# Optimization experiments

Measured on AMD Instinct MI355X. Metric: run time of the kernel, lower is better.

## Reference

```python
import jax, jax.numpy as jnp
import numpy as np

EMBED, ACT, DETER, STOCH, HID = 1536, 10, 2048, 64, 1024
T, B = 64, 256
LN_EPS = 1e-3


def _ln(x, s, b):
    mu = jnp.mean(x, axis=-1, keepdims=True)
    var = jnp.mean(jnp.square(x - mu), axis=-1, keepdims=True)
    return (x - mu) * jax.lax.rsqrt(var + LN_EPS) * s + b


def setup_inputs() -> dict:
    key = jax.random.key(0)
    ks = jax.random.split(key, 20)
    g = lambda k, shp, fan: jax.random.normal(k, shp, jnp.float32) * (1.0 / np.sqrt(fan))
    inp = {
        "embeds": jax.random.normal(ks[0], (T, B, EMBED), jnp.float32),
        "actions": jax.random.normal(ks[1], (T, B, ACT), jnp.float32),
        "h_t": jnp.zeros((B, DETER), jnp.float32),
        "z_t": jnp.zeros((B, STOCH), jnp.float32),
        "noise": jax.random.normal(ks[2], (T, B, STOCH), jnp.float32),
        # DeterNext
        "z_mlp_w": g(ks[3], (HID // 2, STOCH), STOCH),
        "z_mlp_b": jnp.zeros((HID // 2,), jnp.float32),
        "a_mlp_w": g(ks[4], (HID // 2, ACT), ACT),  # bias=False
        "ln_za_s": jnp.ones((HID,), jnp.float32),
        "ln_za_b": jnp.zeros((HID,), jnp.float32),
        # GRUCell (torch layout: [3*deter, in])
        "gru_wih": g(ks[5], (3 * DETER, HID), HID),
        "gru_whh": g(ks[6], (3 * DETER, DETER), DETER),
        "gru_bih": jnp.zeros((3 * DETER,), jnp.float32),
        "gru_bhh": jnp.zeros((3 * DETER,), jnp.float32),
        # PosteriorNext
        "post_h_w": g(ks[7], (HID, DETER), DETER),
        "post_h_b": jnp.zeros((HID,), jnp.float32),
        "post_e_w": g(ks[8], (HID, EMBED), EMBED),
        "post_e_b": jnp.zeros((HID,), jnp.float32),
        "ln_post_s": jnp.ones((HID,), jnp.float32),
        "ln_post_b": jnp.zeros((HID,), jnp.float32),
        "post_w": g(ks[9], (2 * STOCH, HID), HID),
        "post_b": jnp.zeros((2 * STOCH,), jnp.float32),
        # PriorNext
        "prior_h_w": g(ks[10], (HID, DETER), DETER),
        "prior_h_b": jnp.zeros((HID,), jnp.float32),
        "ln_prior_s": jnp.ones((HID,), jnp.float32),
        "ln_prior_b": jnp.zeros((HID,), jnp.float32),
        "prior_w": g(ks[11], (2 * STOCH, HID), HID),
        "prior_b": jnp.zeros((2 * STOCH,), jnp.float32),
    }
    return inp


def _rssm_forward(embeds, actions, h0, z0, noise,
                  z_mlp_w, z_mlp_b, a_mlp_w, ln_za_s, ln_za_b,
                  gru_wih, gru_whh, gru_bih, gru_bhh,
                  post_h_w, post_h_b, post_e_w, post_e_b, ln_post_s, ln_post_b,
                  post_w, post_b,
                  prior_h_w, prior_h_b, ln_prior_s, ln_prior_b, prior_w, prior_b):
    def step(carry, xs):
        h, z = carry
        e, a, n = xs
        # DeterNext: concat(z_mlp(z), a_mlp(a)) -> LN -> ELU
        x = jnp.concatenate([z @ z_mlp_w.T + z_mlp_b, a @ a_mlp_w.T], axis=-1)
        za = jax.nn.elu(_ln(x, ln_za_s, ln_za_b))
        # GRUCell
        gi = za @ gru_wih.T + gru_bih
        gh = h @ gru_whh.T + gru_bhh
        ir, iu, ic = jnp.split(gi, 3, axis=-1)
        hr, hu, hc = jnp.split(gh, 3, axis=-1)
        r = jax.nn.sigmoid(ir + hr)
        u = jax.nn.sigmoid(iu + hu)
        c = jnp.tanh(ic + r * hc)
        h1 = (1.0 - u) * c + u * h
        # PosteriorNext
        p = jax.nn.elu(_ln(h1 @ post_h_w.T + post_h_b + e @ post_e_w.T + post_e_b,
                           ln_post_s, ln_post_b))
        post = p @ post_w.T + post_b  # [B, 2*stoch]
        mean, sraw = jnp.split(post, 2, axis=-1)
        std = 2.0 * jax.nn.sigmoid(sraw) + 0.1
        z1 = mean + std * n  # rsample with externally-supplied noise
        return (h1, z1), (post, h1, z1)

    (_, _), (posts, states_h, post_z_samples) = jax.lax.scan(
        step, (h0, z0), (embeds, actions, noise))
    # batch prior over all timesteps
    pr = jax.nn.elu(_ln(states_h @ prior_h_w.T + prior_h_b, ln_prior_s, ln_prior_b))
    priors = pr @ prior_w.T + prior_b  # [T, B, 2*stoch]
    features = jnp.concatenate([states_h, post_z_samples], axis=-1)  # [T,B,deter+stoch]
    return priors, posts, post_z_samples, features


def reference(embeds, actions, h_t, z_t, noise,
              z_mlp_w, z_mlp_b, a_mlp_w, ln_za_s, ln_za_b,
              gru_wih, gru_whh, gru_bih, gru_bhh,
              post_h_w, post_h_b, post_e_w, post_e_b, ln_post_s, ln_post_b,
              post_w, post_b,
              prior_h_w, prior_h_b, ln_prior_s, ln_prior_b, prior_w, prior_b):
    return _rssm_forward(embeds, actions, h_t, z_t, noise,
                         z_mlp_w, z_mlp_b, a_mlp_w, ln_za_s, ln_za_b,
                         gru_wih, gru_whh, gru_bih, gru_bhh,
                         post_h_w, post_h_b, post_e_w, post_e_b, ln_post_s, ln_post_b,
                         post_w, post_b,
                         prior_h_w, prior_h_b, ln_prior_s, ln_prior_b, prior_w, prior_b)
```

## Files before the change

kernel.cpp:

```cpp
#include <hip/hip_runtime.h>

#define LN_EPS 1e-3f

typedef short s8v __attribute__((ext_vector_type(8)));
typedef float f4v __attribute__((ext_vector_type(4)));
typedef unsigned short u16;

__device__ __forceinline__ u16 f2bf(float f) {
  unsigned int x = __float_as_uint(f);
  x += 0x7fffu + ((x >> 16) & 1u);
  return (u16)(x >> 16);
}
__device__ __forceinline__ float bf2f(u16 u) {
  return __uint_as_float(((unsigned int)u) << 16);
}

__device__ __forceinline__ void glds16(const u16* g, void* l) {
  __builtin_amdgcn_global_load_lds(
      (const __attribute__((address_space(1))) void*)g,
      (__attribute__((address_space(3))) void*)l, 16, 0, 0);
}

__global__ void k_cvt(const float* __restrict__ src, u16* __restrict__ dst, int n) {
  int i = blockIdx.x * blockDim.x + threadIdx.x;
  int stride = gridDim.x * blockDim.x;
  for (; i < n; i += stride) dst[i] = f2bf(src[i]);
}

__global__ void k_packgru(const float* __restrict__ wih,
                          const float* __restrict__ whh, u16* __restrict__ wt) {
  int u = blockIdx.x * 256 + threadIdx.x;
  int nt = u / 73728;
  int r1 = u % 73728;
  int s = r1 / 1536;
  int r2 = r1 % 1536;
  int sub = r2 / 512;
  int r3 = r2 % 512;
  int ch = r3 / 64;
  int row = r3 % 64;
  int j = nt * 64 + row;
  int kbase = s * 64 + ch * 8;
  s8v v;
#pragma unroll
  for (int e = 0; e < 8; ++e) {
    int kk = kbase + e;
    float x;
    if (sub == 0) {
      x = kk < 1024 ? wih[(size_t)j * 1024 + kk] : whh[(size_t)j * 2048 + kk - 1024];
    } else if (sub == 1) {
      int jj = 2048 + j;
      x = kk < 1024 ? wih[(size_t)jj * 1024 + kk] : whh[(size_t)jj * 2048 + kk - 1024];
    } else {
      int jj = 4096 + j;
      x = (s < 16) ? wih[(size_t)jj * 1024 + kk] : whh[(size_t)jj * 2048 + kk - 1024];
    }
    v[e] = (short)f2bf(x);
  }
  *(s8v*)(wt + (size_t)u * 8) = v;
}

__global__ void k_packB(const float* __restrict__ src, u16* __restrict__ dst,
                        int K, int BN, int total) {
  int u = blockIdx.x * 256 + threadIdx.x;
  if (u >= total) return;
  int ns = K >> 6;
  int perNt = ns * 8 * BN;
  int nt = u / perNt;
  int r1 = u % perNt;
  int s = r1 / (8 * BN);
  int r2 = r1 % (8 * BN);
  int ch = r2 / BN;
  int row = r2 % BN;
  int j = nt * BN + row;
  int k = s * 64 + ch * 8;
  const float* sp = src + (size_t)j * K + k;
  s8v v;
#pragma unroll
  for (int e = 0; e < 8; ++e) v[e] = (short)f2bf(sp[e]);
  *(s8v*)(dst + (size_t)u * 8) = v;
}

__global__ void k_hinit(const float* __restrict__ h0, float* __restrict__ hf,
                        u16* __restrict__ acat) {
  int i = blockIdx.x * 256 + threadIdx.x;
  int b = i >> 11, j = i & 2047;
  float v = h0[i];
  hf[i] = v;
  acat[(size_t)b * 3072 + 1024 + j] = f2bf(v);
}

__global__ __launch_bounds__(256) void k_za(
    const float* __restrict__ zsrc, const float* __restrict__ act,
    const float* __restrict__ zw, const float* __restrict__ zb,
    const float* __restrict__ aw, const float* __restrict__ lns,
    const float* __restrict__ lnb, u16* __restrict__ acat) {
  const int b = blockIdx.x, tid = threadIdx.x;
  __shared__ float zsh[64];
  __shared__ float ash[12];
  __shared__ float wred[8];
  if (tid < 64) zsh[tid] = zsrc[b * 64 + tid];
  if (tid < 10) ash[tid] = act[b * 10 + tid];
  __syncthreads();
  float x[4];
#pragma unroll
  for (int i = 0; i < 2; ++i) {
    int c = tid + i * 256;
    const float4* wp = (const float4*)(zw + c * 64);
    float a = zb[c];
#pragma unroll
    for (int k = 0; k < 16; ++k) {
      float4 v = wp[k];
      a += zsh[k * 4] * v.x + zsh[k * 4 + 1] * v.y + zsh[k * 4 + 2] * v.z +
           zsh[k * 4 + 3] * v.w;
    }
    x[i] = a;
  }
#pragma unroll
  for (int i = 2; i < 4; ++i) {
    int c2 = tid + (i - 2) * 256;
    const float* wp = aw + c2 * 10;
    float a = 0.f;
#pragma unroll
    for (int k = 0; k < 10; ++k) a += ash[k] * wp[k];
    x[i] = a;
  }
  float s = x[0] + x[1] + x[2] + x[3];
#pragma unroll
  for (int o = 1; o < 64; o <<= 1) s += __shfl_xor(s, o);
  if ((tid & 63) == 0) wred[tid >> 6] = s;
  __syncthreads();
  float mu = (wred[0] + wred[1] + wred[2] + wred[3]) * (1.f / 1024.f);
  float q = 0.f;
#pragma unroll
  for (int i = 0; i < 4; ++i) {
    float d = x[i] - mu;
    q += d * d;
  }
#pragma unroll
  for (int o = 1; o < 64; o <<= 1) q += __shfl_xor(q, o);
  if ((tid & 63) == 0) wred[4 + (tid >> 6)] = q;
  __syncthreads();
  float rs = rsqrtf((wred[4] + wred[5] + wred[6] + wred[7]) * (1.f / 1024.f) + LN_EPS);
  int cols[4] = {tid, tid + 256, 512 + tid, 768 + tid};
#pragma unroll
  for (int i = 0; i < 4; ++i) {
    int c = cols[i];
    float y = (x[i] - mu) * rs * lns[c] + lnb[c];
    y = y > 0.f ? y : expm1f(y);
    acat[(size_t)b * 3072 + c] = f2bf(y);
  }
}

__global__ __launch_bounds__(256) void k_gru(
    const u16* __restrict__ acat_r, const u16* __restrict__ wt,
    const float* __restrict__ bih, const float* __restrict__ bhh,
    const float* __restrict__ hf_r, float* __restrict__ hf_w,
    u16* __restrict__ acat_w, float* __restrict__ feat, int t) {
  const int hw = blockIdx.x;
  const int logical = (hw & 7) * 32 + (hw >> 3);
  const int mg = logical & 7;
  const int nt = logical >> 3;
  const int m0 = mg * 32;
  const int tid = threadIdx.x;
  const int lane = tid & 63;
  const int w = tid >> 6;
  const int lr = lane & 15, lk = lane >> 4;

  __shared__ __align__(16) char smem[2][28672];

  const int arow = 8 * w + (lane >> 3);
  const int acol8 = ((lane & 7) ^ (arow & 7)) * 8;
  const u16* aSrc = acat_r + (size_t)(m0 + arow) * 3072 + acol8;
  const u16* wtNt = wt + (size_t)nt * 48 * 3 * 4096;

  f4v accr[2], accu[2], acci[2], acch[2];
  accr[0] = accr[1] = accu[0] = accu[1] = (f4v)(0.f);
  acci[0] = acci[1] = acch[0] = acch[1] = (f4v)(0.f);

#define K1_STAGE(BB, S) { \
    char* base = &smem[BB][0]; \
    glds16(aSrc + (S) * 64, base + w * 1024); \
    const u16* bsrc = wtNt + (size_t)(S) * 3 * 4096; \
    _Pragma("unroll") for (int i = 0; i < 6; ++i) { \
      int cf = w + i * 4; \
      glds16(bsrc + (cf * 64 + lane) * 8, base + 4096 + cf * 1024); \
    } }

#define K1_COMP(BB, ACCX) { \
    char* base = &smem[BB][0]; \
    _Pragma("unroll") for (int kk = 0; kk < 2; ++kk) { \
      int ch = kk * 4 + lk; \
      int r0 = lr, r1 = 16 + lr; \
      s8v a0 = *(const s8v*)(base + r0 * 128 + ((ch ^ (r0 & 7)) * 16)); \
      s8v a1 = *(const s8v*)(base + r1 * 128 + ((ch ^ (r1 & 7)) * 16)); \
      int rb = (w * 16 + lr) * 16; \
      s8v br = *(const s8v*)(base + 4096 + ch * 1024 + rb); \
      s8v bu = *(const s8v*)(base + 12288 + ch * 1024 + rb); \
      s8v bx = *(const s8v*)(base + 20480 + ch * 1024 + rb); \
      accr[0] = __builtin_amdgcn_mfma_f32_16x16x32_bf16(a0, br, accr[0], 0, 0, 0); \
      accr[1] = __builtin_amdgcn_mfma_f32_16x16x32_bf16(a1, br, accr[1], 0, 0, 0); \
      accu[0] = __builtin_amdgcn_mfma_f32_16x16x32_bf16(a0, bu, accu[0], 0, 0, 0); \
      accu[1] = __builtin_amdgcn_mfma_f32_16x16x32_bf16(a1, bu, accu[1], 0, 0, 0); \
      ACCX[0] = __builtin_amdgcn_mfma_f32_16x16x32_bf16(a0, bx, ACCX[0], 0, 0, 0); \
      ACCX[1] = __builtin_amdgcn_mfma_f32_16x16x32_bf16(a1, bx, ACCX[1], 0, 0, 0); \
    } }

  K1_STAGE(0, 0)
  int buf = 0;
  for (int s = 0; s < 16; ++s) {
    asm volatile("s_waitcnt vmcnt(0)" ::: "memory");
    __builtin_amdgcn_s_barrier();
    __builtin_amdgcn_sched_barrier(0);
    K1_STAGE(buf ^ 1, s + 1)
    K1_COMP(buf, acci)
    buf ^= 1;
  }
  for (int s = 16; s < 48; ++s) {
    asm volatile("s_waitcnt vmcnt(0)" ::: "memory");
    __builtin_amdgcn_s_barrier();
    __builtin_amdgcn_sched_barrier(0);
    if (s + 1 < 48) K1_STAGE(buf ^ 1, s + 1)
    K1_COMP(buf, acch)
    buf ^= 1;
  }

  const int j = nt * 64 + w * 16 + lr;
  const float b_ri = bih[j], b_rh = bhh[j];
  const float b_ui = bih[2048 + j], b_uh = bhh[2048 + j];
  const float b_ci = bih[4096 + j], b_ch = bhh[4096 + j];
#pragma unroll
  for (int m = 0; m < 2; ++m) {
#pragma unroll
    for (int r = 0; r < 4; ++r) {
      int grow = m0 + m * 16 + lk * 4 + r;
      float vr = accr[m][r] + b_ri + b_rh;
      float vu = accu[m][r] + b_ui + b_uh;
      float ic = acci[m][r] + b_ci;
      float hc = acch[m][r] + b_ch;
      float rg = 1.f / (1.f + expf(-vr));
      float ug = 1.f / (1.f + expf(-vu));
      float c = tanhf(ic + rg * hc);
      float hold = hf_r[(size_t)grow * 2048 + j];
      float h1 = (1.f - ug) * c + ug * hold;
      hf_w[(size_t)grow * 2048 + j] = h1;
      acat_w[(size_t)grow * 3072 + 1024 + j] = f2bf(h1);
      feat[(size_t)(t * 256 + grow) * 2112 + j] = h1;
    }
  }
#undef K1_STAGE
#undef K1_COMP
}

__global__ __launch_bounds__(256) void k_post(
    const u16* __restrict__ acat_h, const u16* __restrict__ wp,
    const float* __restrict__ bias, const u16* __restrict__ epart_t,
    float* __restrict__ xbuf) {
  const int bx = blockIdx.x;
  const int mg = bx & 7, nt = bx >> 3;
  const int m0 = mg * 32;
  const int tid = threadIdx.x;
  const int lane = tid & 63;
  const int w = tid >> 6;
  const int lr = lane & 15, lk = lane >> 4;

  __shared__ __align__(16) char smem[2][12288];

  const int arow = 8 * w + (lane >> 3);
  const int acol8 = ((lane & 7) ^ (arow & 7)) * 8;
  const u16* aSrc = acat_h + (size_t)(m0 + arow) * 3072 + 1024 + acol8;
  const u16* wpNt = wp + (size_t)nt * 32 * 4096;

  f4v acc[2];
  acc[0] = (f4v)(0.f);
  acc[1] = (f4v)(0.f);

#define K2_STAGE(BB, S) { \
    char* base = &smem[BB][0]; \
    glds16(aSrc + (S) * 64, base + w * 1024); \
    const u16* bsrc = wpNt + (size_t)(S) * 4096; \
    _Pragma("unroll") for (int i = 0; i < 2; ++i) { \
      int cf = w + i * 4; \
      glds16(bsrc + (cf * 64 + lane) * 8, base + 4096 + cf * 1024); \
    } }

  K2_STAGE(0, 0)
  int buf = 0;
  for (int s = 0; s < 32; ++s) {
    asm volatile("s_waitcnt vmcnt(0)" ::: "memory");
    __builtin_amdgcn_s_barrier();
    __builtin_amdgcn_sched_barrier(0);
    if (s + 1 < 32) K2_STAGE(buf ^ 1, s + 1)
    char* base = &smem[buf][0];
#pragma unroll
    for (int kk = 0; kk < 2; ++kk) {
      int ch = kk * 4 + lk;
      int r0 = lr, r1 = 16 + lr;
      s8v a0 = *(const s8v*)(base + r0 * 128 + ((ch ^ (r0 & 7)) * 16));
      s8v a1 = *(const s8v*)(base + r1 * 128 + ((ch ^ (r1 & 7)) * 16));
      s8v b = *(const s8v*)(base + 4096 + ch * 1024 + (w * 16 + lr) * 16);
      acc[0] = __builtin_amdgcn_mfma_f32_16x16x32_bf16(a0, b, acc[0], 0, 0, 0);
      acc[1] = __builtin_amdgcn_mfma_f32_16x16x32_bf16(a1, b, acc[1], 0, 0, 0);
    }
    buf ^= 1;
  }
  const int col = nt * 64 + w * 16 + lr;
#pragma unroll
  for (int m = 0; m < 2; ++m) {
#pragma unroll
    for (int r = 0; r < 4; ++r) {
      int grow = m0 + m * 16 + lk * 4 + r;
      float v = acc[m][r] + bias[col] + bf2f(epart_t[(size_t)grow * 1024 + col]);
      xbuf[(size_t)grow * 1024 + col] = v;
    }
  }
#undef K2_STAGE
}

__global__ __launch_bounds__(512) void k_postz(
    const float* __restrict__ xb, const u16* __restrict__ pw,
    const float* __restrict__ lns, const float* __restrict__ lnb,
    const float* __restrict__ pb, float* __restrict__ posts_t,
    const float* __restrict__ noise_t, float* __restrict__ zout,
    float* __restrict__ feat, int t) {
  const int m0 = blockIdx.x * 32;
  const int tid = threadIdx.x;
  const int lane = tid & 63;
  const int w = tid >> 6;
  const int lr = lane & 15, lk = lane >> 4;
  __shared__ __align__(16) u16 As[2][32][64];
  __shared__ __align__(16) u16 Bs[2][8][128][8];
  __shared__ float lmu[32], lrs[32];
  __shared__ float ps[32][132];
  {
    int row = tid >> 4, sg = tid & 15;
    const float4* xp = (const float4*)(xb + (size_t)(m0 + row) * 1024 + sg * 64);
    float s = 0.f, q = 0.f;
#pragma unroll
    for (int i = 0; i < 16; ++i) {
      float4 v = xp[i];
      s += v.x + v.y + v.z + v.w;
      q += v.x * v.x + v.y * v.y + v.z * v.z + v.w * v.w;
    }
#pragma unroll
    for (int o = 1; o < 16; o <<= 1) {
      s += __shfl_xor(s, o);
      q += __shfl_xor(q, o);
    }
    if (sg == 0) {
      float mu = s * (1.f / 1024.f);
      lmu[row] = mu;
      lrs[row] = rsqrtf(q * (1.f / 1024.f) - mu * mu + LN_EPS);
    }
  }
  __syncthreads();

#define K3_STAGEA(BB, S) if (tid < 256) { \
    int row = tid >> 3, k8 = tid & 7; \
    const float* xp = xb + (size_t)(m0 + row) * 1024 + (S) * 64 + k8 * 8; \
    float mu = lmu[row], rs = lrs[row]; \
    s8v v; \
    _Pragma("unroll") for (int e = 0; e < 8; ++e) { \
      int c = (S) * 64 + k8 * 8 + e; \
      float y = (xp[e] - mu) * rs * lns[c] + lnb[c]; \
      y = y > 0.f ? y : expm1f(y); \
      v[e] = (short)f2bf(y); \
    } \
    *(s8v*)((char*)&As[BB][0][0] + row * 128 + ((k8 ^ (row & 7)) * 16)) = v; }

#define K3_STAGEB(BB, S) { \
    const u16* bsrc = pw + (size_t)(S) * 8192; \
    glds16(bsrc + (((w >> 1) * 128 + (w & 1) * 64 + lane) * 8), \
           (char*)&Bs[BB][0][0][0] + w * 1024); \
    glds16(bsrc + ((((w >> 1) + 4) * 128 + (w & 1) * 64 + lane) * 8), \
           (char*)&Bs[BB][0][0][0] + w * 1024 + 8192); }

  f4v acc[2];
  acc[0] = (f4v)(0.f);
  acc[1] = (f4v)(0.f);
  K3_STAGEA(0, 0)
  K3_STAGEB(0, 0)
  __syncthreads();
  int buf = 0;
  for (int s = 0; s < 16; ++s) {
    if (s + 1 < 16) {
      K3_STAGEA(buf ^ 1, s + 1)
      K3_STAGEB(buf ^ 1, s + 1)
    }
#pragma unroll
    for (int kk = 0; kk < 2; ++kk) {
      int ch = kk * 4 + lk;
      int r0 = lr, r1 = 16 + lr;
      s8v a0 = *(const s8v*)((char*)&As[buf][0][0] + r0 * 128 + ((ch ^ (r0 & 7)) * 16));
      s8v a1 = *(const s8v*)((char*)&As[buf][0][0] + r1 * 128 + ((ch ^ (r1 & 7)) * 16));
      s8v b = *(const s8v*)((char*)&Bs[buf][0][0][0] + ch * 2048 + (w * 16 + lr) * 16);
      acc[0] = __builtin_amdgcn_mfma_f32_16x16x32_bf16(a0, b, acc[0], 0, 0, 0);
      acc[1] = __builtin_amdgcn_mfma_f32_16x16x32_bf16(a1, b, acc[1], 0, 0, 0);
    }
    __syncthreads();
    buf ^= 1;
  }
#pragma unroll
  for (int m = 0; m < 2; ++m) {
#pragma unroll
    for (int r = 0; r < 4; ++r) {
      int row = m * 16 + lk * 4 + r;
      int col = w * 16 + lr;
      float v = acc[m][r] + pb[col];
      posts_t[(size_t)(m0 + row) * 128 + col] = v;
      ps[row][col] = v;
    }
  }
  __syncthreads();
#pragma unroll
  for (int q = 0; q < 4; ++q) {
    int e = q * 512 + tid;
    int row = e >> 6, j = e & 63;
    float mean = ps[row][j], sraw = ps[row][64 + j];
    float sd = 2.f / (1.f + expf(-sraw)) + 0.1f;
    float z = mean + sd * noise_t[(m0 + row) * 64 + j];
    zout[(m0 + row) * 64 + j] = z;
    feat[(size_t)(t * 256 + m0 + row) * 2112 + 2048 + j] = z;
  }
#undef K3_STAGEA
#undef K3_STAGEB
}

template <bool AF32, bool OUTBF16>
__global__ __launch_bounds__(512) void k_gemm8(
    const void* __restrict__ Av, int lda, const u16* __restrict__ Bw, int ldb,
    int nstage, float* __restrict__ Cf, u16* __restrict__ Cb, int ldc,
    const float* __restrict__ bias) {
  const int bx = blockIdx.x, by = blockIdx.y;
  const int tid = threadIdx.x;
  const int m0 = bx * 64;
  const int n0 = by * 128;
  __shared__ __align__(16) u16 As[64][72];
  __shared__ __align__(16) u16 Bs[128][72];
  const int lane = tid & 63;
  const int w = tid >> 6;
  const int wr = w >> 2;
  const int wc = w & 3;
  const int lr = lane & 15;
  const int lk = lane >> 4;

  f4v acc[2][2];
#pragma unroll
  for (int m = 0; m < 2; ++m)
#pragma unroll
    for (int n = 0; n < 2; ++n) acc[m][n] = (f4v)(0.0f);

  for (int s = 0; s < nstage; ++s) {
    const int k0 = s << 6;
    {
      int row = tid >> 3, k8 = (tid & 7) << 3;
      if (AF32) {
        const float* ap = (const float*)Av + (size_t)(m0 + row) * lda + k0 + k8;
        float4 f0 = *(const float4*)ap;
        float4 f1 = *(const float4*)(ap + 4);
        s8v v;
        v[0] = (short)f2bf(f0.x); v[1] = (short)f2bf(f0.y);
        v[2] = (short)f2bf(f0.z); v[3] = (short)f2bf(f0.w);
        v[4] = (short)f2bf(f1.x); v[5] = (short)f2bf(f1.y);
        v[6] = (short)f2bf(f1.z); v[7] = (short)f2bf(f1.w);
        *(s8v*)&As[row][k8] = v;
      } else {
        *(s8v*)&As[row][k8] =
            *(const s8v*)((const u16*)Av + (size_t)(m0 + row) * lda + k0 + k8);
      }
    }
#pragma unroll
    for (int it = 0; it < 2; ++it) {
      int c = tid + it * 512;
      int row = c >> 3, k8 = (c & 7) << 3;
      *(s8v*)&Bs[row][k8] = *(const s8v*)(Bw + (size_t)(n0 + row) * ldb + k0 + k8);
    }
    __syncthreads();
#pragma unroll
    for (int kk = 0; kk < 2; ++kk) {
      const int koff = kk * 32 + lk * 8;
      s8v a[2], b[2];
      a[0] = *(const s8v*)&As[wr * 32 + lr][koff];
      a[1] = *(const s8v*)&As[wr * 32 + 16 + lr][koff];
      b[0] = *(const s8v*)&Bs[wc * 32 + lr][koff];
      b[1] = *(const s8v*)&Bs[wc * 32 + 16 + lr][koff];
#pragma unroll
      for (int m = 0; m < 2; ++m)
#pragma unroll
        for (int n = 0; n < 2; ++n)
          acc[m][n] =
              __builtin_amdgcn_mfma_f32_16x16x32_bf16(a[m], b[n], acc[m][n], 0, 0, 0);
    }
    __syncthreads();
  }
#pragma unroll
  for (int m = 0; m < 2; ++m) {
#pragma unroll
    for (int n = 0; n < 2; ++n) {
#pragma unroll
      for (int r = 0; r < 4; ++r) {
        int row = m0 + wr * 32 + m * 16 + lk * 4 + r;
        int col = n0 + wc * 32 + n * 16 + lr;
        float v = acc[m][n][r];
        if (bias) v += bias[col];
        if (OUTBF16)
          Cb[(size_t)row * ldc + col] = f2bf(v);
        else
          Cf[(size_t)row * ldc + col] = v;
      }
    }
  }
}

__global__ __launch_bounds__(256) void k_lnelu(const u16* __restrict__ xsrc,
                                               const float* __restrict__ s,
                                               const float* __restrict__ bb,
                                               u16* __restrict__ out) {
  int row = blockIdx.x, tid = threadIdx.x;
  __shared__ float red[256];
  float v[4];
#pragma unroll
  for (int i = 0; i < 4; ++i) {
    size_t idx = (size_t)row * 1024 + tid + i * 256;
    v[i] = bf2f(xsrc[idx]);
  }
  float sm = v[0] + v[1] + v[2] + v[3];
  red[tid] = sm;
  __syncthreads();
  for (int o = 128; o > 0; o >>= 1) {
    if (tid < o) red[tid] += red[tid + o];
    __syncthreads();
  }
  float mu = red[0] * (1.0f / 1024.0f);
  __syncthreads();
  float q = 0.f;
#pragma unroll
  for (int i = 0; i < 4; ++i) {
    float d = v[i] - mu;
    q += d * d;
  }
  red[tid] = q;
  __syncthreads();
  for (int o = 128; o > 0; o >>= 1) {
    if (tid < o) red[tid] += red[tid + o];
    __syncthreads();
  }
  float rs = rsqrtf(red[0] * (1.0f / 1024.0f) + LN_EPS);
#pragma unroll
  for (int i = 0; i < 4; ++i) {
    int c = tid + i * 256;
    float y = (v[i] - mu) * rs * s[c] + bb[c];
    y = y > 0.f ? y : expm1f(y);
    out[(size_t)row * 1024 + c] = f2bf(y);
  }
}

extern "C" void kernel_launch(void* const* d_in, const int* in_sizes, int n_in,
                              void* d_out, int out_size, void* d_ws,
                              size_t ws_size, hipStream_t stream) {
  const float* embeds = (const float*)d_in[0];
  const float* actions = (const float*)d_in[1];
  const float* h_t = (const float*)d_in[2];
  const float* z_t = (const float*)d_in[3];
  const float* noise = (const float*)d_in[4];
  const float* z_mlp_w = (const float*)d_in[5];
  const float* z_mlp_b = (const float*)d_in[6];
  const float* a_mlp_w = (const float*)d_in[7];
  const float* ln_za_s = (const float*)d_in[8];
  const float* ln_za_b = (const float*)d_in[9];
  const float* gru_wih = (const float*)d_in[10];
  const float* gru_whh = (const float*)d_in[11];
  const float* gru_bih = (const float*)d_in[12];
  const float* gru_bhh = (const float*)d_in[13];
  const float* post_h_w = (const float*)d_in[14];
  const float* post_h_b = (const float*)d_in[15];
  const float* post_e_w = (const float*)d_in[16];
  const float* post_e_b = (const float*)d_in[17];
  const float* ln_post_s = (const float*)d_in[18];
  const float* ln_post_b = (const float*)d_in[19];
  const float* post_w = (const float*)d_in[20];
  const float* post_b = (const float*)d_in[21];
  const float* prior_h_w = (const float*)d_in[22];
  const float* prior_h_b = (const float*)d_in[23];
  const float* ln_prior_s = (const float*)d_in[24];
  const float* ln_prior_b = (const float*)d_in[25];
  const float* prior_w = (const float*)d_in[26];
  const float* prior_b = (const float*)d_in[27];

  float* out = (float*)d_out;
  float* out_priors = out;
  float* out_posts = out + 2097152;
  float* out_z = out + 4194304;
  float* out_feat = out + 5242880;

  char* ws = (char*)d_ws;
  size_t off = 0;
  auto alloc = [&](size_t bytes) {
    char* p = ws + off;
    off += (bytes + 255) & ~(size_t)255;
    return p;
  };
  char* regW = alloc((size_t)32 * 48 * 3 * 4096 * 2);
  u16* wt = (u16*)regW;
  u16* prx_b = (u16*)regW;
  u16* posthP = (u16*)alloc((size_t)1024 * 2048 * 2);
  u16* postwP = (u16*)alloc((size_t)128 * 1024 * 2);
  u16* poste_b = (u16*)alloc((size_t)1024 * 1536 * 2);
  u16* priorh_b = (u16*)alloc((size_t)1024 * 2048 * 2);
  u16* priorw_b = (u16*)alloc((size_t)128 * 1024 * 2);
  u16* acat0 = (u16*)alloc((size_t)256 * 3072 * 2);
  u16* acat1 = (u16*)alloc((size_t)256 * 3072 * 2);
  float* hf0 = (float*)alloc((size_t)256 * 2048 * 4);
  float* hf1 = (float*)alloc((size_t)256 * 2048 * 4);
  float* xbuf = (float*)alloc((size_t)256 * 1024 * 4);
  char* regU = alloc((size_t)16384 * 1024 * 2);
  u16* e_part = (u16*)regU;
  u16* p_pr = (u16*)regU;

  u16* acat[2] = {acat0, acat1};
  float* hf[2] = {hf0, hf1};

  k_packgru<<<9216, 256, 0, stream>>>(gru_wih, gru_whh, wt);
  k_packB<<<1024, 256, 0, stream>>>(post_h_w, posthP, 2048, 64, 262144);
  k_packB<<<64, 256, 0, stream>>>(post_w, postwP, 1024, 128, 16384);
  k_cvt<<<512, 256, 0, stream>>>(post_e_w, poste_b, 1024 * 1536);
  k_cvt<<<512, 256, 0, stream>>>(prior_h_w, priorh_b, 1024 * 2048);
  k_cvt<<<64, 256, 0, stream>>>(prior_w, priorw_b, 128 * 1024);
  k_hinit<<<2048, 256, 0, stream>>>(h_t, hf0, acat0);

  k_gemm8<true, true><<<dim3(256, 8), 512, 0, stream>>>(
      embeds, 1536, poste_b, 1536, 24, nullptr, e_part, 1024, post_e_b);

  for (int t = 0; t < 64; ++t) {
    const int rI = t & 1, wI = rI ^ 1;
    const float* zsrc = (t == 0) ? z_t : (out_z + (size_t)(t - 1) * 16384);
    k_za<<<256, 256, 0, stream>>>(zsrc, actions + (size_t)t * 2560, z_mlp_w,
                                  z_mlp_b, a_mlp_w, ln_za_s, ln_za_b, acat[rI]);
    k_gru<<<256, 256, 0, stream>>>(acat[rI], wt, gru_bih, gru_bhh, hf[rI],
                                   hf[wI], acat[wI], out_feat, t);
    k_post<<<128, 256, 0, stream>>>(acat[wI], posthP, post_h_b,
                                    e_part + (size_t)t * 262144, xbuf);
    k_postz<<<8, 512, 0, stream>>>(xbuf, postwP, ln_post_s, ln_post_b, post_b,
                                   out_posts + (size_t)t * 32768,
                                   noise + (size_t)t * 16384,
                                   out_z + (size_t)t * 16384, out_feat, t);
  }

  k_gemm8<true, true><<<dim3(256, 8), 512, 0, stream>>>(
      out_feat, 2112, priorh_b, 2048, 32, nullptr, prx_b, 1024, prior_h_b);
  k_lnelu<<<16384, 256, 0, stream>>>(prx_b, ln_prior_s, ln_prior_b, p_pr);
  k_gemm8<false, false><<<dim3(256, 1), 512, 0, stream>>>(
      p_pr, 1024, priorw_b, 1024, 16, out_priors, nullptr, 128, prior_b);
}
```

Before: 7.119 ms.

## Fuse z/action MLP with LayerNorm into GRU kernel and pipeline staging

Removes the separate k_za launch per timestep. Each GRU block now recomputes the z/action projection and its LayerNorm+ELU for its 32 rows directly into LDS, and the h-part of the GRU weights is streamed first so the recomputation overlaps the loads. The GRU weight packing is reordered (whh before wih), blocks use 512 threads with one accumulator set per wave, and the post kernels switch to deeper vmcnt-based double buffering with raw barriers. The cost is redundant z-MLP computation across the 32 N-tile blocks, a one-pass variance formula with lower numerical accuracy, and a larger LDS footprint.

After: 16.83 ms. 2.36x slower.

```diff
diff --git a/kernel.cpp b/kernel.cpp
--- a/kernel.cpp
+++ b/kernel.cpp
@@ -20,6 +20,13 @@
       (const __attribute__((address_space(1))) void*)g,
       (__attribute__((address_space(3))) void*)l, 16, 0, 0);
 }
+__device__ __forceinline__ void glds4(const u16* g, void* l) {
+  __builtin_amdgcn_global_load_lds(
+      (const __attribute__((address_space(1))) void*)g,
+      (__attribute__((address_space(3))) void*)l, 4, 0, 0);
+}
+
+#define RAW_BAR() do { __builtin_amdgcn_s_barrier(); __builtin_amdgcn_sched_barrier(0); } while (0)
 
 __global__ void k_cvt(const float* __restrict__ src, u16* __restrict__ dst, int n) {
   int i = blockIdx.x * blockDim.x + threadIdx.x;
@@ -38,21 +45,15 @@
   int r3 = r2 % 512;
   int ch = r3 / 64;
   int row = r3 % 64;
-  int j = nt * 64 + row;
-  int kbase = s * 64 + ch * 8;
+  int j = sub * 2048 + nt * 64 + row;
   s8v v;
 #pragma unroll
   for (int e = 0; e < 8; ++e) {
-    int kk = kbase + e;
     float x;
-    if (sub == 0) {
-      x = kk < 1024 ? wih[(size_t)j * 1024 + kk] : whh[(size_t)j * 2048 + kk - 1024];
-    } else if (sub == 1) {
-      int jj = 2048 + j;
-      x = kk < 1024 ? wih[(size_t)jj * 1024 + kk] : whh[(size_t)jj * 2048 + kk - 1024];
+    if (s < 32) {
+      x = whh[(size_t)j * 2048 + s * 64 + ch * 8 + e];
     } else {
-      int jj = 4096 + j;
-      x = (s < 16) ? wih[(size_t)jj * 1024 + kk] : whh[(size_t)jj * 2048 + kk - 1024];
+      x = wih[(size_t)j * 1024 + (s - 32) * 64 + ch * 8 + e];
     }
     v[e] = (short)f2bf(x);
   }
@@ -81,81 +82,22 @@
 }
 
 __global__ void k_hinit(const float* __restrict__ h0, float* __restrict__ hf,
-                        u16* __restrict__ acat) {
+                        u16* __restrict__ hcat) {
   int i = blockIdx.x * 256 + threadIdx.x;
-  int b = i >> 11, j = i & 2047;
   float v = h0[i];
   hf[i] = v;
-  acat[(size_t)b * 3072 + 1024 + j] = f2bf(v);
-}
-
-__global__ __launch_bounds__(256) void k_za(
+  hcat[i] = f2bf(v);
+}
+
+__global__ __launch_bounds__(512) void k_gru(
     const float* __restrict__ zsrc, const float* __restrict__ act,
     const float* __restrict__ zw, const float* __restrict__ zb,
-    const float* __restrict__ aw, const float* __restrict__ lns,
-    const float* __restrict__ lnb, u16* __restrict__ acat) {
-  const int b = blockIdx.x, tid = threadIdx.x;
-  __shared__ float zsh[64];
-  __shared__ float ash[12];
-  __shared__ float wred[8];
-  if (tid < 64) zsh[tid] = zsrc[b * 64 + tid];
-  if (tid < 10) ash[tid] = act[b * 10 + tid];
-  __syncthreads();
-  float x[4];
-#pragma unroll
-  for (int i = 0; i < 2; ++i) {
-    int c = tid + i * 256;
-    const float4* wp = (const float4*)(zw + c * 64);
-    float a = zb[c];
-#pragma unroll
-    for (int k = 0; k < 16; ++k) {
-      float4 v = wp[k];
-      a += zsh[k * 4] * v.x + zsh[k * 4 + 1] * v.y + zsh[k * 4 + 2] * v.z +
-           zsh[k * 4 + 3] * v.w;
-    }
-    x[i] = a;
-  }
-#pragma unroll
-  for (int i = 2; i < 4; ++i) {
-    int c2 = tid + (i - 2) * 256;
-    const float* wp = aw + c2 * 10;
-    float a = 0.f;
-#pragma unroll
-    for (int k = 0; k < 10; ++k) a += ash[k] * wp[k];
-    x[i] = a;
-  }
-  float s = x[0] + x[1] + x[2] + x[3];
-#pragma unroll
-  for (int o = 1; o < 64; o <<= 1) s += __shfl_xor(s, o);
-  if ((tid & 63) == 0) wred[tid >> 6] = s;
-  __syncthreads();
-  float mu = (wred[0] + wred[1] + wred[2] + wred[3]) * (1.f / 1024.f);
-  float q = 0.f;
-#pragma unroll
-  for (int i = 0; i < 4; ++i) {
-    float d = x[i] - mu;
-    q += d * d;
-  }
-#pragma unroll
-  for (int o = 1; o < 64; o <<= 1) q += __shfl_xor(q, o);
-  if ((tid & 63) == 0) wred[4 + (tid >> 6)] = q;
-  __syncthreads();
-  float rs = rsqrtf((wred[4] + wred[5] + wred[6] + wred[7]) * (1.f / 1024.f) + LN_EPS);
-  int cols[4] = {tid, tid + 256, 512 + tid, 768 + tid};
-#pragma unroll
-  for (int i = 0; i < 4; ++i) {
-    int c = cols[i];
-    float y = (x[i] - mu) * rs * lns[c] + lnb[c];
-    y = y > 0.f ? y : expm1f(y);
-    acat[(size_t)b * 3072 + c] = f2bf(y);
-  }
-}
-
-__global__ __launch_bounds__(256) void k_gru(
-    const u16* __restrict__ acat_r, const u16* __restrict__ wt,
-    const float* __restrict__ bih, const float* __restrict__ bhh,
-    const float* __restrict__ hf_r, float* __restrict__ hf_w,
-    u16* __restrict__ acat_w, float* __restrict__ feat, int t) {
+    const float* __restrict__ aw, const float* __restrict__ lnzs,
+    const float* __restrict__ lnzb, const u16* __restrict__ hcat_r,
+    const u16* __restrict__ wt, const float* __restrict__ bih,
+    const float* __restrict__ bhh, const float* __restrict__ hf_r,
+    float* __restrict__ hf_w, u16* __restrict__ hcat_w,
+    float* __restrict__ feat, int t) {
   const int hw = blockIdx.x;
   const int logical = (hw & 7) * 32 + (hw >> 3);
   const int mg = logical & 7;
@@ -165,98 +107,177 @@
   const int lane = tid & 63;
   const int w = tid >> 6;
   const int lr = lane & 15, lk = lane >> 4;
-
-  __shared__ __align__(16) char smem[2][28672];
-
-  const int arow = 8 * w + (lane >> 3);
-  const int acol8 = ((lane & 7) ^ (arow & 7)) * 8;
-  const u16* aSrc = acat_r + (size_t)(m0 + arow) * 3072 + acol8;
-  const u16* wtNt = wt + (size_t)nt * 48 * 3 * 4096;
-
-  f4v accr[2], accu[2], acci[2], acch[2];
-  accr[0] = accr[1] = accu[0] = accu[1] = (f4v)(0.f);
-  acci[0] = acci[1] = acch[0] = acch[1] = (f4v)(0.f);
-
-#define K1_STAGE(BB, S) { \
-    char* base = &smem[BB][0]; \
-    glds16(aSrc + (S) * 64, base + w * 1024); \
-    const u16* bsrc = wtNt + (size_t)(S) * 3 * 4096; \
-    _Pragma("unroll") for (int i = 0; i < 6; ++i) { \
-      int cf = w + i * 4; \
-      glds16(bsrc + (cf * 64 + lane) * 8, base + 4096 + cf * 1024); \
+  const int mh = w & 1, cs = w >> 1;
+
+  __shared__ __align__(16) char bufs[2][28672];
+  __shared__ __align__(16) char zals[16][4096];
+
+  const u16* wtNt = wt + (size_t)nt * 48 * 12288;
+
+  const int q0 = w * 2, q1 = w * 2 + 1;
+  const int row0 = q0 * 2 + (lane >> 5), row1 = q1 * 2 + (lane >> 5);
+  const int slot = (lane & 31) >> 2, b4 = lane & 3;
+  const u16* aS0 = hcat_r + (size_t)(m0 + row0) * 2048 +
+                   ((slot ^ (row0 & 7)) << 3) + (b4 << 1);
+  const u16* aS1 = hcat_r + (size_t)(m0 + row1) * 2048 +
+                   ((slot ^ (row1 & 7)) << 3) + (b4 << 1);
+
+  f4v accr = (f4v)(0.f), accu = (f4v)(0.f), acci = (f4v)(0.f), acch = (f4v)(0.f);
+
+#define K1_STAGEH(BB, S) { \
+    char* base = &bufs[BB][0]; \
+    glds4(aS0 + (S) * 64, base + q0 * 256); \
+    glds4(aS1 + (S) * 64, base + q1 * 256); \
+    const u16* bsrc = wtNt + (size_t)(S) * 12288; \
+    _Pragma("unroll") for (int j = 0; j < 3; ++j) { \
+      int c = w + j * 8; \
+      glds16(bsrc + c * 512 + lane * 8, base + 4096 + c * 1024); \
     } }
 
-#define K1_COMP(BB, ACCX) { \
-    char* base = &smem[BB][0]; \
+#define K1_STAGEZ(BB, S) { \
+    char* base = &bufs[BB][0]; \
+    const u16* bsrc = wtNt + (size_t)(S) * 12288; \
+    _Pragma("unroll") for (int j = 0; j < 3; ++j) { \
+      int c = w + j * 8; \
+      glds16(bsrc + c * 512 + lane * 8, base + 4096 + c * 1024); \
+    } }
+
+#define K1_COMP(BB, ABASE, ACCX) { \
+    char* base = &bufs[BB][0]; \
     _Pragma("unroll") for (int kk = 0; kk < 2; ++kk) { \
       int ch = kk * 4 + lk; \
-      int r0 = lr, r1 = 16 + lr; \
-      s8v a0 = *(const s8v*)(base + r0 * 128 + ((ch ^ (r0 & 7)) * 16)); \
-      s8v a1 = *(const s8v*)(base + r1 * 128 + ((ch ^ (r1 & 7)) * 16)); \
-      int rb = (w * 16 + lr) * 16; \
-      s8v br = *(const s8v*)(base + 4096 + ch * 1024 + rb); \
-      s8v bu = *(const s8v*)(base + 12288 + ch * 1024 + rb); \
-      s8v bx = *(const s8v*)(base + 20480 + ch * 1024 + rb); \
-      accr[0] = __builtin_amdgcn_mfma_f32_16x16x32_bf16(a0, br, accr[0], 0, 0, 0); \
-      accr[1] = __builtin_amdgcn_mfma_f32_16x16x32_bf16(a1, br, accr[1], 0, 0, 0); \
-      accu[0] = __builtin_amdgcn_mfma_f32_16x16x32_bf16(a0, bu, accu[0], 0, 0, 0); \
-      accu[1] = __builtin_amdgcn_mfma_f32_16x16x32_bf16(a1, bu, accu[1], 0, 0, 0); \
-      ACCX[0] = __builtin_amdgcn_mfma_f32_16x16x32_bf16(a0, bx, ACCX[0], 0, 0, 0); \
-      ACCX[1] = __builtin_amdgcn_mfma_f32_16x16x32_bf16(a1, bx, ACCX[1], 0, 0, 0); \
+      int r = mh * 16 + lr; \
+      s8v a = *(const s8v*)((ABASE) + r * 128 + ((ch ^ (r & 7)) << 4)); \
+      int boff = 4096 + ch * 1024 + ((cs * 16 + lr) << 4); \
+      s8v br = *(const s8v*)(base + boff); \
+      s8v bu = *(const s8v*)(base + boff + 8192); \
+      s8v bx = *(const s8v*)(base + boff + 16384); \
+      accr = __builtin_amdgcn_mfma_f32_16x16x32_bf16(a, br, accr, 0, 0, 0); \
+      accu = __builtin_amdgcn_mfma_f32_16x16x32_bf16(a, bu, accu, 0, 0, 0); \
+      ACCX = __builtin_amdgcn_mfma_f32_16x16x32_bf16(a, bx, ACCX, 0, 0, 0); \
     } }
 
-  K1_STAGE(0, 0)
-  int buf = 0;
-  for (int s = 0; s < 16; ++s) {
+  K1_STAGEH(0, 0)
+  {
+    const int zrow = tid >> 4, g = tid & 15;
+    const int grow = m0 + zrow;
+    char* zbase = &zals[0][0] + zrow * 128;
+    float4 zv[16];
+    const float4* zp = (const float4*)(zsrc + grow * 64);
+#pragma unroll
+    for (int k = 0; k < 16; ++k) zv[k] = zp[k];
+    float sacc = 0.f, qacc = 0.f;
+#pragma unroll 1
+    for (int cc = 0; cc < 32; ++cc) {
+      int c = g * 32 + cc;
+      const float4* wp = (const float4*)(zw + c * 64);
+      float a = zb[c];
+#pragma unroll
+      for (int k = 0; k < 16; ++k) {
+        float4 wv = wp[k];
+        a += zv[k].x * wv.x + zv[k].y * wv.y + zv[k].z * wv.z + zv[k].w * wv.w;
+      }
+      sacc += a;
+      qacc += a * a;
+      *(u16*)(zbase + (c >> 6) * 4096 + ((((c >> 3) & 7) ^ (zrow & 7)) << 4) +
+              ((c & 7) << 1)) = f2bf(a);
+    }
+    float av[10];
+#pragma unroll
+    for (int k = 0; k < 10; ++k) av[k] = act[grow * 10 + k];
+#pragma unroll 1
+    for (int cc = 0; cc < 32; ++cc) {
+      int c2 = g * 32 + cc;
+      const float* ap = aw + c2 * 10;
+      float a = 0.f;
+#pragma unroll
+      for (int k = 0; k < 10; ++k) a += av[k] * ap[k];
+      sacc += a;
+      qacc += a * a;
+      int c = 512 + c2;
+      *(u16*)(zbase + (c >> 6) * 4096 + ((((c >> 3) & 7) ^ (zrow & 7)) << 4) +
+              ((c & 7) << 1)) = f2bf(a);
+    }
+#pragma unroll
+    for (int o = 1; o < 16; o <<= 1) {
+      sacc += __shfl_xor(sacc, o);
+      qacc += __shfl_xor(qacc, o);
+    }
+    float mu = sacc * (1.f / 1024.f);
+    float rs = rsqrtf(qacc * (1.f / 1024.f) - mu * mu + LN_EPS);
+#pragma unroll 1
+    for (int cc = 0; cc < 64; ++cc) {
+      int c = (cc < 32) ? (g * 32 + cc) : (512 + g * 32 + cc - 32);
+      u16* p = (u16*)(zbase + (c >> 6) * 4096 +
+                      ((((c >> 3) & 7) ^ (zrow & 7)) << 4) + ((c & 7) << 1));
+      float x = bf2f(*p);
+      float y = (x - mu) * rs * lnzs[c] + lnzb[c];
+      y = y > 0.f ? y : expm1f(y);
+      *p = f2bf(y);
+    }
+  }
+  asm volatile("s_waitcnt lgkmcnt(0)" ::: "memory");
+  RAW_BAR();
+
+  for (int s = 0; s < 31; ++s) {
+    K1_STAGEH((s + 1) & 1, s + 1)
+    asm volatile("s_waitcnt vmcnt(5)" ::: "memory");
+    RAW_BAR();
+    K1_COMP(s & 1, &bufs[s & 1][0], acch)
+    RAW_BAR();
+  }
+  {
+    K1_STAGEZ(0, 32)
+    asm volatile("s_waitcnt vmcnt(3)" ::: "memory");
+    RAW_BAR();
+    K1_COMP(1, &bufs[1][0], acch)
+    RAW_BAR();
+  }
+  for (int s = 32; s < 47; ++s) {
+    K1_STAGEZ((s + 1) & 1, s + 1)
+    asm volatile("s_waitcnt vmcnt(3)" ::: "memory");
+    RAW_BAR();
+    K1_COMP(s & 1, &zals[s - 32][0], acci)
+    RAW_BAR();
+  }
+  {
     asm volatile("s_waitcnt vmcnt(0)" ::: "memory");
-    __builtin_amdgcn_s_barrier();
-    __builtin_amdgcn_sched_barrier(0);
-    K1_STAGE(buf ^ 1, s + 1)
-    K1_COMP(buf, acci)
-    buf ^= 1;
-  }
-  for (int s = 16; s < 48; ++s) {
-    asm volatile("s_waitcnt vmcnt(0)" ::: "memory");
-    __builtin_amdgcn_s_barrier();
-    __builtin_amdgcn_sched_barrier(0);
-    if (s + 1 < 48) K1_STAGE(buf ^ 1, s + 1)
-    K1_COMP(buf, acch)
-    buf ^= 1;
-  }
-
-  const int j = nt * 64 + w * 16 + lr;
-  const float b_ri = bih[j], b_rh = bhh[j];
-  const float b_ui = bih[2048 + j], b_uh = bhh[2048 + j];
-  const float b_ci = bih[4096 + j], b_ch = bhh[4096 + j];
-#pragma unroll
-  for (int m = 0; m < 2; ++m) {
-#pragma unroll
-    for (int r = 0; r < 4; ++r) {
-      int grow = m0 + m * 16 + lk * 4 + r;
-      float vr = accr[m][r] + b_ri + b_rh;
-      float vu = accu[m][r] + b_ui + b_uh;
-      float ic = acci[m][r] + b_ci;
-      float hc = acch[m][r] + b_ch;
-      float rg = 1.f / (1.f + expf(-vr));
-      float ug = 1.f / (1.f + expf(-vu));
-      float c = tanhf(ic + rg * hc);
-      float hold = hf_r[(size_t)grow * 2048 + j];
-      float h1 = (1.f - ug) * c + ug * hold;
-      hf_w[(size_t)grow * 2048 + j] = h1;
-      acat_w[(size_t)grow * 3072 + 1024 + j] = f2bf(h1);
-      feat[(size_t)(t * 256 + grow) * 2112 + j] = h1;
-    }
-  }
-#undef K1_STAGE
+    RAW_BAR();
+    K1_COMP(1, &zals[15][0], acci)
+  }
+
+  const int col = nt * 64 + cs * 16 + lr;
+  const float b_ri = bih[col], b_rh = bhh[col];
+  const float b_ui = bih[2048 + col], b_uh = bhh[2048 + col];
+  const float b_ci = bih[4096 + col], b_ch = bhh[4096 + col];
+#pragma unroll
+  for (int r = 0; r < 4; ++r) {
+    int grow = m0 + mh * 16 + lk * 4 + r;
+    float vr = accr[r] + b_ri + b_rh;
+    float vu = accu[r] + b_ui + b_uh;
+    float ic = acci[r] + b_ci;
+    float hc = acch[r] + b_ch;
+    float rg = 1.f / (1.f + expf(-vr));
+    float ug = 1.f / (1.f + expf(-vu));
+    float c = tanhf(ic + rg * hc);
+    float hold = hf_r[(size_t)grow * 2048 + col];
+    float h1 = (1.f - ug) * c + ug * hold;
+    hf_w[(size_t)grow * 2048 + col] = h1;
+    hcat_w[(size_t)grow * 2048 + col] = f2bf(h1);
+    feat[(size_t)(t * 256 + grow) * 2112 + col] = h1;
+  }
+#undef K1_STAGEH
+#undef K1_STAGEZ
 #undef K1_COMP
 }
 
 __global__ __launch_bounds__(256) void k_post(
-    const u16* __restrict__ acat_h, const u16* __restrict__ wp,
+    const u16* __restrict__ hcat, const u16* __restrict__ wp,
     const float* __restrict__ bias, const u16* __restrict__ epart_t,
     float* __restrict__ xbuf) {
-  const int bx = blockIdx.x;
-  const int mg = bx & 7, nt = bx >> 3;
+  const int hw = blockIdx.x;
+  const int logical = (hw & 7) * 16 + (hw >> 3);
+  const int mg = logical & 7, nt = logical >> 3;
   const int m0 = mg * 32;
   const int tid = threadIdx.x;
   const int lane = tid & 63;
@@ -267,7 +288,7 @@
 
   const int arow = 8 * w + (lane >> 3);
   const int acol8 = ((lane & 7) ^ (arow & 7)) * 8;
-  const u16* aSrc = acat_h + (size_t)(m0 + arow) * 3072 + 1024 + acol8;
+  const u16* aSrc = hcat + (size_t)(m0 + arow) * 2048 + acol8;
   const u16* wpNt = wp + (size_t)nt * 32 * 4096;
 
   f4v acc[2];
@@ -283,25 +304,30 @@
       glds16(bsrc + (cf * 64 + lane) * 8, base + 4096 + cf * 1024); \
     } }
 
+#define K2_COMP(BB) { \
+    char* base = &smem[BB][0]; \
+    _Pragma("unroll") for (int kk = 0; kk < 2; ++kk) { \
+      int ch = kk * 4 + lk; \
+      int r0 = lr, r1 = 16 + lr; \
+      s8v a0 = *(const s8v*)(base + r0 * 128 + ((ch ^ (r0 & 7)) * 16)); \
+      s8v a1 = *(const s8v*)(base + r1 * 128 + ((ch ^ (r1 & 7)) * 16)); \
+      s8v b = *(const s8v*)(base + 4096 + ch * 1024 + (w * 16 + lr) * 16); \
+      acc[0] = __builtin_amdgcn_mfma_f32_16x16x32_bf16(a0, b, acc[0], 0, 0, 0); \
+      acc[1] = __builtin_amdgcn_mfma_f32_16x16x32_bf16(a1, b, acc[1], 0, 0, 0); \
+    } }
+
   K2_STAGE(0, 0)
-  int buf = 0;
-  for (int s = 0; s < 32; ++s) {
+  for (int s = 0; s < 31; ++s) {
+    K2_STAGE((s + 1) & 1, s + 1)
+    asm volatile("s_waitcnt vmcnt(3)" ::: "memory");
+    RAW_BAR();
+    K2_COMP(s & 1)
+    RAW_BAR();
+  }
+  {
     asm volatile("s_waitcnt vmcnt(0)" ::: "memory");
-    __builtin_amdgcn_s_barrier();
-    __builtin_amdgcn_sched_barrier(0);
-    if (s + 1 < 32) K2_STAGE(buf ^ 1, s + 1)
-    char* base = &smem[buf][0];
-#pragma unroll
-    for (int kk = 0; kk < 2; ++kk) {
-      int ch = kk * 4 + lk;
-      int r0 = lr, r1 = 16 + lr;
-      s8v a0 = *(const s8v*)(base + r0 * 128 + ((ch ^ (r0 & 7)) * 16));
-      s8v a1 = *(const s8v*)(base + r1 * 128 + ((ch ^ (r1 & 7)) * 16));
-      s8v b = *(const s8v*)(base + 4096 + ch * 1024 + (w * 16 + lr) * 16);
-      acc[0] = __builtin_amdgcn_mfma_f32_16x16x32_bf16(a0, b, acc[0], 0, 0, 0);
-      acc[1] = __builtin_amdgcn_mfma_f32_16x16x32_bf16(a1, b, acc[1], 0, 0, 0);
-    }
-    buf ^= 1;
+    RAW_BAR();
+    K2_COMP(1)
   }
   const int col = nt * 64 + w * 16 + lr;
 #pragma unroll
@@ -314,6 +340,7 @@
     }
   }
 #undef K2_STAGE
+#undef K2_COMP
 }
 
 __global__ __launch_bounds__(512) void k_postz(
@@ -379,13 +406,16 @@
   acc[1] = (f4v)(0.f);
   K3_STAGEA(0, 0)
   K3_STAGEB(0, 0)
-  __syncthreads();
   int buf = 0;
   for (int s = 0; s < 16; ++s) {
     if (s + 1 < 16) {
       K3_STAGEA(buf ^ 1, s + 1)
       K3_STAGEB(buf ^ 1, s + 1)
-    }
+      asm volatile("s_waitcnt vmcnt(2) lgkmcnt(0)" ::: "memory");
+    } else {
+      asm volatile("s_waitcnt vmcnt(0) lgkmcnt(0)" ::: "memory");
+    }
+    RAW_BAR();
 #pragma unroll
     for (int kk = 0; kk < 2; ++kk) {
       int ch = kk * 4 + lk;
@@ -396,7 +426,7 @@
       acc[0] = __builtin_amdgcn_mfma_f32_16x16x32_bf16(a0, b, acc[0], 0, 0, 0);
       acc[1] = __builtin_amdgcn_mfma_f32_16x16x32_bf16(a1, b, acc[1], 0, 0, 0);
     }
-    __syncthreads();
+    __builtin_amdgcn_s_barrier();
     buf ^= 1;
   }
 #pragma unroll
@@ -599,7 +629,7 @@
     off += (bytes + 255) & ~(size_t)255;
     return p;
   };
-  char* regW = alloc((size_t)32 * 48 * 3 * 4096 * 2);
+  char* regW = alloc((size_t)32 * 48 * 12288 * 2);
   u16* wt = (u16*)regW;
   u16* prx_b = (u16*)regW;
   u16* posthP = (u16*)alloc((size_t)1024 * 2048 * 2);
@@ -607,8 +637,8 @@
   u16* poste_b = (u16*)alloc((size_t)1024 * 1536 * 2);
   u16* priorh_b = (u16*)alloc((size_t)1024 * 2048 * 2);
   u16* priorw_b = (u16*)alloc((size_t)128 * 1024 * 2);
-  u16* acat0 = (u16*)alloc((size_t)256 * 3072 * 2);
-  u16* acat1 = (u16*)alloc((size_t)256 * 3072 * 2);
+  u16* hcat0 = (u16*)alloc((size_t)256 * 2048 * 2);
+  u16* hcat1 = (u16*)alloc((size_t)256 * 2048 * 2);
   float* hf0 = (float*)alloc((size_t)256 * 2048 * 4);
   float* hf1 = (float*)alloc((size_t)256 * 2048 * 4);
   float* xbuf = (float*)alloc((size_t)256 * 1024 * 4);
@@ -616,7 +646,7 @@
   u16* e_part = (u16*)regU;
   u16* p_pr = (u16*)regU;
 
-  u16* acat[2] = {acat0, acat1};
+  u16* hcat[2] = {hcat0, hcat1};
   float* hf[2] = {hf0, hf1};
 
   k_packgru<<<9216, 256, 0, stream>>>(gru_wih, gru_whh, wt);
@@ -625,7 +655,7 @@
   k_cvt<<<512, 256, 0, stream>>>(post_e_w, poste_b, 1024 * 1536);
   k_cvt<<<512, 256, 0, stream>>>(prior_h_w, priorh_b, 1024 * 2048);
   k_cvt<<<64, 256, 0, stream>>>(prior_w, priorw_b, 128 * 1024);
-  k_hinit<<<2048, 256, 0, stream>>>(h_t, hf0, acat0);
+  k_hinit<<<2048, 256, 0, stream>>>(h_t, hf0, hcat0);
 
   k_gemm8<true, true><<<dim3(256, 8), 512, 0, stream>>>(
       embeds, 1536, poste_b, 1536, 24, nullptr, e_part, 1024, post_e_b);
@@ -633,11 +663,11 @@
   for (int t = 0; t < 64; ++t) {
     const int rI = t & 1, wI = rI ^ 1;
     const float* zsrc = (t == 0) ? z_t : (out_z + (size_t)(t - 1) * 16384);
-    k_za<<<256, 256, 0, stream>>>(zsrc, actions + (size_t)t * 2560, z_mlp_w,
-                                  z_mlp_b, a_mlp_w, ln_za_s, ln_za_b, acat[rI]);
-    k_gru<<<256, 256, 0, stream>>>(acat[rI], wt, gru_bih, gru_bhh, hf[rI],
-                                   hf[wI], acat[wI], out_feat, t);
-    k_post<<<128, 256, 0, stream>>>(acat[wI], posthP, post_h_b,
+    k_gru<<<256, 512, 0, stream>>>(zsrc, actions + (size_t)t * 2560, z_mlp_w,
+                                   z_mlp_b, a_mlp_w, ln_za_s, ln_za_b,
+                                   hcat[rI], wt, gru_bih, gru_bhh, hf[rI],
+                                   hf[wI], hcat[wI], out_feat, t);
+    k_post<<<128, 256, 0, stream>>>(hcat[wI], posthP, post_h_b,
                                     e_part + (size_t)t * 262144, xbuf);
     k_postz<<<8, 512, 0, stream>>>(xbuf, postwP, ln_post_s, ln_post_b, post_b,
                                    out_posts + (size_t)t * 32768,
```
